# Kernel optimization log

Measured on AMD Instinct MI355X. Metric: run time of the kernel, lower is better.

Reference implementation:

```python
import jax, jax.numpy as jnp
import numpy as np

NEG_INF = -jnp.inf


def _rope(x, cos, sin):
    # x: (B, S, H, D); cos/sin: (1, S, 1, D//2)
    xr = x.reshape(*x.shape[:-1], -1, 2)
    x1, x2 = xr[..., 0], xr[..., 1]  # (B, S, H, D//2) each
    # faithful to source: concat halves along last axis, same total size D
    return jnp.concatenate([x1 * cos - x2 * sin, x1 * sin + x2 * cos], axis=-1)


def setup_inputs() -> dict:
    B, S, D, H, Ld = 2, 2048, 2048, 16, 128
    key = jax.random.key(0)
    ks = jax.random.split(key, 6)
    sc = 1.0 / np.sqrt(D)
    return {
        "x": jax.random.normal(ks[0], (B, S, D), jnp.float32),
        "attn_mask": jnp.ones((B, S), jnp.int32),
        "Wq": jax.random.normal(ks[1], (D, H * Ld), jnp.float32) * sc,
        "bq": jnp.zeros((H * Ld,), jnp.float32),
        "Wk": jax.random.normal(ks[2], (D, H * Ld), jnp.float32) * sc,
        "bk": jnp.zeros((H * Ld,), jnp.float32),
        "Wv": jax.random.normal(ks[3], (D, H * Ld), jnp.float32) * sc,
        "bv": jnp.zeros((H * Ld,), jnp.float32),
        "Wo": jax.random.normal(ks[4], (H * Ld, D), jnp.float32) * sc,
        "bo": jnp.zeros((D,), jnp.float32),
        "num_heads": H,
    }


def reference(x, attn_mask, Wq, bq, Wk, bk, Wv, bv, Wo, bo, num_heads):
    B, S, D = x.shape
    H = int(num_heads)
    Ld = Wq.shape[1] // H
    base = 10000

    q = (x @ Wq + bq).reshape(B, S, H, Ld)
    k = (x @ Wk + bk).reshape(B, S, H, Ld)
    v = (x @ Wv + bv).reshape(B, S, H, Ld)

    # rotary tables (match RotaryEmbedding.setup, sliced to seq_len)
    inv_freq = 1.0 / base ** (2 * jnp.arange(0, Ld // 2) / Ld)
    angles = jnp.arange(S)[:, None] * inv_freq[None, :]  # (S, Ld//2)
    cos = jnp.cos(angles)[None, :, None, :].astype(x.dtype)
    sin = jnp.sin(angles)[None, :, None, :].astype(x.dtype)
    q = _rope(q, cos, sin)
    k = _rope(k, cos, sin)

    q = jnp.transpose(q, (0, 2, 1, 3))  # (B, H, S, Ld)
    k = jnp.transpose(k, (0, 2, 1, 3))
    v = jnp.transpose(v, (0, 2, 1, 3))

    scale = jnp.sqrt(jnp.float32(Ld)).astype(x.dtype)
    scores = jnp.einsum('bnqd,bnkd->bnqk', q, k) / scale  # (B, H, S, S)

    # faithful mask from source: keep where arange[None,:] >= arange[:,None]
    row_idx = jnp.arange(S)[None, :]
    col_idx = jnp.arange(S)[:, None]
    keep = row_idx >= col_idx  # (S, S)
    scores = jnp.where(keep[None, None, :, :], scores, NEG_INF)

    # padding mask applied over the QUERY axis, as in source: (B,1,S,1)
    scores = jnp.where(attn_mask[:, None, :, None] > 0, scores, NEG_INF)

    attn = jax.nn.softmax(scores, axis=-1)
    attended = jnp.einsum('bnqk,bnkd->bnqd', attn, v)
    attended = jnp.transpose(attended, (0, 2, 1, 3)).reshape(B, S, H * Ld)
    return attended @ Wo + bo
```

## Files before the change

### kernel.cpp

```cpp
#include <hip/hip_runtime.h>
#include <math.h>

typedef __bf16 bf16x8 __attribute__((ext_vector_type(8)));
typedef float f32x4 __attribute__((ext_vector_type(4)));

#define MFMA_BF16(a,b,c) __builtin_amdgcn_mfma_f32_16x16x32_bf16((a),(b),(c),0,0,0)

static constexpr int S_LEN = 2048;
static constexpr int DM    = 2048;
static constexpr int NHEAD = 16;
static constexpr int LDH   = 128;
static constexpr int BATCH = 2;
static constexpr size_t QKV_SEG = (size_t)BATCH * NHEAD * S_LEN * LDH;

__device__ __forceinline__ unsigned short f2bf(float f) {
    unsigned u = __float_as_uint(f);
    u += 0x7fffu + ((u >> 16) & 1u);
    return (unsigned short)(u >> 16);
}
__device__ __forceinline__ float bf2f(unsigned short h) {
    return __uint_as_float(((unsigned)h) << 16);
}
__device__ __forceinline__ float fexp2(float x) { return exp2f(x); }

__device__ __forceinline__ void ld_lds16(const void* g, void* l) {
    __builtin_amdgcn_global_load_lds(
        (const __attribute__((address_space(1))) unsigned int*)g,
        (__attribute__((address_space(3))) unsigned int*)l, 16, 0, 0);
}

__global__ void convert_f32_bf16(const float* __restrict__ in,
                                 unsigned short* __restrict__ out, int n4) {
    int idx = blockIdx.x * blockDim.x + threadIdx.x;
    if (idx >= n4) return;
    float4 v = reinterpret_cast<const float4*>(in)[idx];
    unsigned lo = (unsigned)f2bf(v.x) | ((unsigned)f2bf(v.y) << 16);
    unsigned hi = (unsigned)f2bf(v.z) | ((unsigned)f2bf(v.w) << 16);
    reinterpret_cast<uint2*>(out)[idx] = make_uint2(lo, hi);
}

__global__ void gen_tab(float* __restrict__ ct, float* __restrict__ st) {
    int i = threadIdx.x & 63;
    int s = blockIdx.x * 4 + (threadIdx.x >> 6);
    float freq = (float)exp(-(double)(2 * i) / 128.0 * 9.210340371976184);
    float a = (float)s * freq;
    ct[s * 64 + i] = cosf(a);
    st[s * 64 + i] = sinf(a);
}

__global__ void wconv_t4(const float* __restrict__ W0, const float* __restrict__ W1,
                         const float* __restrict__ W2, const float* __restrict__ W3,
                         unsigned short* __restrict__ O0, unsigned short* __restrict__ O1,
                         unsigned short* __restrict__ O2, unsigned short* __restrict__ O3) {
    __shared__ unsigned short tile[32][33];
    int z = blockIdx.z;
    const float* W = (z == 0) ? W0 : (z == 1) ? W1 : (z == 2) ? W2 : W3;
    unsigned short* Wt = (z == 0) ? O0 : (z == 1) ? O1 : (z == 2) ? O2 : O3;
    int n0 = blockIdx.x * 32;
    int k0 = blockIdx.y * 32;
    int t = threadIdx.x;
    int ir = t >> 3, ic = (t & 7) * 4;
    float4 v = *reinterpret_cast<const float4*>(&W[(size_t)(k0 + ir) * DM + n0 + ic]);
    tile[ir][ic + 0] = f2bf(v.x);
    tile[ir][ic + 1] = f2bf(v.y);
    tile[ir][ic + 2] = f2bf(v.z);
    tile[ir][ic + 3] = f2bf(v.w);
    __syncthreads();
    unsigned lo = (unsigned)tile[ic + 0][ir] | ((unsigned)tile[ic + 1][ir] << 16);
    unsigned hi = (unsigned)tile[ic + 2][ir] | ((unsigned)tile[ic + 3][ir] << 16);
    *reinterpret_cast<uint2*>(&Wt[(size_t)(n0 + ir) * DM + k0 + ic]) = make_uint2(lo, hi);
}

template<int MODE>
__global__ __launch_bounds__(256, 2) void gemm_bf16(
    const unsigned short* __restrict__ A,
    const unsigned short* __restrict__ Bt,
    const float* __restrict__ b0, const float* __restrict__ b1,
    const float* __restrict__ b2,
    const float* __restrict__ ctab, const float* __restrict__ stab,
    void* __restrict__ outp)
{
    const int K = DM;
    constexpr int SMEM_SHORTS = (MODE == 0) ? 16384 : 8192;
    __shared__ __attribute__((aligned(16))) unsigned short smem[SMEM_SHORTS];
    unsigned short* As = smem;
    unsigned short* Bs = smem + 4096;
    int t = threadIdx.x;
    int m0 = blockIdx.y * 128, n0 = blockIdx.x * 128;
    int lane = t & 63, i16 = lane & 15, quad = lane >> 4;
    int w = t >> 6;
    int wm = (w >> 1) * 64, wn = (w & 1) * 64;

    f32x4 acc[4][4];
    const f32x4 z4 = {0.f, 0.f, 0.f, 0.f};
    for (int mi = 0; mi < 4; ++mi)
        for (int ni = 0; ni < 4; ++ni) acc[mi][ni] = z4;

    for (int kk = 0; kk < K; kk += 32) {
        __syncthreads();
#pragma unroll
        for (int j = 0; j < 2; ++j) {
            int off = j * 4096 + w * 1024 + lane * 16;
            int row = off >> 6;
            int g = ((off >> 4) & 3) ^ ((row >> 1) & 3);
            ld_lds16(&A [(size_t)(m0 + row) * K + kk + g * 8], (char*)As + off);
            ld_lds16(&Bt[(size_t)(n0 + row) * K + kk + g * 8], (char*)Bs + off);
        }
        __syncthreads();

        bf16x8 aF[4], bF[4];
#pragma unroll
        for (int mi = 0; mi < 4; ++mi) {
            int rA = wm + mi * 16 + i16;
            aF[mi] = *reinterpret_cast<const bf16x8*>(
                (const char*)As + rA * 64 + ((quad ^ ((rA >> 1) & 3)) * 16));
        }
#pragma unroll
        for (int ni = 0; ni < 4; ++ni) {
            int rB = wn + ni * 16 + i16;
            bF[ni] = *reinterpret_cast<const bf16x8*>(
                (const char*)Bs + rB * 64 + ((quad ^ ((rB >> 1) & 3)) * 16));
        }
#pragma unroll
        for (int mi = 0; mi < 4; ++mi)
#pragma unroll
            for (int ni = 0; ni < 4; ++ni)
                acc[mi][ni] = MFMA_BF16(aF[mi], bF[ni], acc[mi][ni]);
    }

    if constexpr (MODE == 0) {
        unsigned short* Cs = smem;
        __syncthreads();
        int which = n0 >> 11;
        int hh = (n0 & (DM - 1)) >> 7;
        const float* bp = (which == 0) ? b0 : ((which == 1) ? b1 : b2);
        if (which == 2) {
            for (int mi = 0; mi < 4; ++mi)
                for (int ni = 0; ni < 4; ++ni) {
                    int d = wn + ni * 16 + i16;
                    float bv = bp[(n0 & (DM - 1)) + d];
                    for (int r = 0; r < 4; ++r) {
                        int sl = wm + mi * 16 + quad * 4 + r;
                        Cs[d * 128 + (((sl >> 3) ^ (d & 15)) * 8) + (sl & 7)] =
                            f2bf(acc[mi][ni][r] + bv);
                    }
                }
            __syncthreads();
            int s0 = m0 & (S_LEN - 1), bb = m0 >> 11;
            unsigned short* vout = (unsigned short*)outp + 2 * QKV_SEG;
#pragma unroll
            for (int it = 0; it < 8; ++it) {
                int idx = it * 256 + t;
                int d = idx >> 4, sg = idx & 15;
                uint4 v = *reinterpret_cast<const uint4*>(&Cs[d * 128 + ((sg ^ (d & 15)) * 8)]);
                size_t oidx = (((size_t)(bb * NHEAD + hh)) * LDH + d) * S_LEN + s0 + sg * 8;
                *reinterpret_cast<uint4*>(vout + oidx) = v;
            }
        } else {
            for (int mi = 0; mi < 4; ++mi)
                for (int ni = 0; ni < 4; ++ni) {
                    int nl = wn + ni * 16 + i16;
                    float bv = bp[(n0 & (DM - 1)) + nl];
                    for (int r = 0; r < 4; ++r) {
                        int ml = wm + mi * 16 + quad * 4 + r;
                        Cs[ml * 128 + nl] = f2bf(acc[mi][ni][r] + bv);
                    }
                }
            __syncthreads();
            float qscale = (which == 0) ? (0.08838834764831845f * 1.4426950408889634f) : 1.0f;
            unsigned short* qout = (unsigned short*)outp + (size_t)which * QKV_SEG;
#pragma unroll
            for (int it = 0; it < 8; ++it) {
                int idx = it * 256 + t;
                int row = idx >> 4, c16 = idx & 15;
                int mm = m0 + row;
                int ss = mm & (S_LEN - 1), bb = mm >> 11;
                int i8 = (c16 & 7) * 8;
                const unsigned short* crow = Cs + row * 128 + i8 * 2;
                uint4 w0 = *reinterpret_cast<const uint4*>(crow);
                uint4 w1 = *reinterpret_cast<const uint4*>(crow + 8);
                unsigned pw[8] = {w0.x, w0.y, w0.z, w0.w, w1.x, w1.y, w1.z, w1.w};
                float4 cA = *reinterpret_cast<const float4*>(&ctab[ss * 64 + i8]);
                float4 cB = *reinterpret_cast<const float4*>(&ctab[ss * 64 + i8 + 4]);
                float4 sA = *reinterpret_cast<const float4*>(&stab[ss * 64 + i8]);
                float4 sB = *reinterpret_cast<const float4*>(&stab[ss * 64 + i8 + 4]);
                float cv[8] = {cA.x, cA.y, cA.z, cA.w, cB.x, cB.y, cB.z, cB.w};
                float sv[8] = {sA.x, sA.y, sA.z, sA.w, sB.x, sB.y, sB.z, sB.w};
                bool hi = (c16 >= 8);
                unsigned short ov[8];
#pragma unroll
                for (int j = 0; j < 8; ++j) {
                    float xe = bf2f((unsigned short)(pw[j] & 0xffff));
                    float xo = bf2f((unsigned short)(pw[j] >> 16));
                    float o = hi ? (xe * sv[j] + xo * cv[j]) : (xe * cv[j] - xo * sv[j]);
                    ov[j] = f2bf(o * qscale);
                }
                size_t oidx = (((size_t)(bb * NHEAD + hh)) * S_LEN + ss) * LDH + c16 * 8;
                *reinterpret_cast<uint4*>(qout + oidx) =
                    *reinterpret_cast<const uint4*>(ov);
            }
        }
    } else {
        for (int mi = 0; mi < 4; ++mi) {
            for (int ni = 0; ni < 4; ++ni) {
                int nn = n0 + wn + ni * 16 + i16;
                float bv = b0[nn];
                for (int r = 0; r < 4; ++r) {
                    int mm = m0 + wm + mi * 16 + quad * 4 + r;
                    ((float*)outp)[(size_t)mm * DM + nn] = acc[mi][ni][r] + bv;
                }
            }
        }
    }
}

__global__ __launch_bounds__(256, 2) void attn_kernel(
    const unsigned short* __restrict__ q,
    const unsigned short* __restrict__ k,
    const unsigned short* __restrict__ vt,
    unsigned short* __restrict__ att)
{
    __shared__ __attribute__((aligned(16))) unsigned short Ks[2][64 * 128];
    __shared__ __attribute__((aligned(16))) unsigned short Vs[2][128 * 64];
    __shared__ __attribute__((aligned(16))) unsigned short Ps[4][32 * 64];

    int bid = blockIdx.x;
    int second = bid >> 8;
    int p = bid & 255;
    int xb = second ? (15 - (p >> 5)) : (p >> 5);
    int bh = p & 31;
    int b = bh >> 4, h = bh & (NHEAD - 1);
    int q0 = xb * 128;

    int t = threadIdx.x, w = t >> 6, lane = t & 63;
    int i16 = lane & 15, quad = lane >> 4;
    int qbase = q0 + w * 32;

    bf16x8 qf[2][4];
#pragma unroll
    for (int qs = 0; qs < 2; ++qs) {
        const unsigned short* qrow = q + ((size_t)bh * S_LEN + qbase + qs * 16 + i16) * LDH;
#pragma unroll
        for (int c = 0; c < 4; ++c)
            qf[qs][c] = *reinterpret_cast<const bf16x8*>(qrow + c * 32 + quad * 8);
    }

    const f32x4 z4 = {0.f, 0.f, 0.f, 0.f};
    f32x4 o[2][8];
#pragma unroll
    for (int qs = 0; qs < 2; ++qs)
#pragma unroll
        for (int dt = 0; dt < 8; ++dt) o[qs][dt] = z4;
    float l_i[2] = {0.f, 0.f};

    const unsigned short* kbh  = k  + (size_t)bh * S_LEN * LDH;
    const unsigned short* vtbh = vt + (size_t)bh * LDH * S_LEN;
    unsigned short* PsW = Ps[w];

    auto stage = [&](int buf, int kk0) {
#pragma unroll
        for (int j = 0; j < 4; ++j) {
            int off = j * 4096 + w * 1024 + lane * 16;
            int key = off >> 8;
            int gk = ((off >> 4) & 15) ^ (key & 15);
            ld_lds16(&kbh[(size_t)(kk0 + key) * LDH + gk * 8], (char*)Ks[buf] + off);
            int d = off >> 7;
            int gv = ((off >> 4) & 7) ^ (d & 7);
            ld_lds16(&vtbh[(size_t)d * S_LEN + kk0 + gv * 8], (char*)Vs[buf] + off);
        }
    };

    stage(0, q0);
    int nch = (S_LEN - q0) >> 6;
    for (int ci = 0; ci < nch; ++ci) {
        __syncthreads();
        if (ci + 1 < nch) stage((ci + 1) & 1, q0 + (ci + 1) * 64);
        int kk0 = q0 + ci * 64;
        if (kk0 + 64 <= qbase) continue;
        const unsigned short* Kb = Ks[ci & 1];
        const unsigned short* Vb = Vs[ci & 1];

        f32x4 s[2][4];
#pragma unroll
        for (int qs = 0; qs < 2; ++qs)
#pragma unroll
            for (int kn = 0; kn < 4; ++kn) s[qs][kn] = z4;
#pragma unroll
        for (int c = 0; c < 4; ++c) {
            bf16x8 kf[4];
#pragma unroll
            for (int kn = 0; kn < 4; ++kn) {
                int key = kn * 16 + i16;
                int gs = (c * 4 + quad) ^ (key & 15);
                kf[kn] = *reinterpret_cast<const bf16x8*>((const char*)Kb + key * 256 + gs * 16);
            }
#pragma unroll
            for (int qs = 0; qs < 2; ++qs)
#pragma unroll
                for (int kn = 0; kn < 4; ++kn)
                    s[qs][kn] = MFMA_BF16(kf[kn], qf[qs][c], s[qs][kn]);
        }

        bool diag = (kk0 < qbase + 32);
#pragma unroll
        for (int qs = 0; qs < 2; ++qs) {
            int q_local = qs * 16 + i16;
            int qg = qbase + q_local;
#pragma unroll
            for (int kn = 0; kn < 4; ++kn) {
                int keyb = kk0 + kn * 16 + quad * 4;
                float pv[4];
                if (diag) {
#pragma unroll
                    for (int r = 0; r < 4; ++r)
                        pv[r] = (keyb + r >= qg) ? fexp2(s[qs][kn][r]) : 0.f;
                } else {
#pragma unroll
                    for (int r = 0; r < 4; ++r) pv[r] = fexp2(s[qs][kn][r]);
                }
                l_i[qs] += (pv[0] + pv[1]) + (pv[2] + pv[3]);
                unsigned lo = (unsigned)f2bf(pv[0]) | ((unsigned)f2bf(pv[1]) << 16);
                unsigned hi = (unsigned)f2bf(pv[2]) | ((unsigned)f2bf(pv[3]) << 16);
                int g = (kn * 2 + (quad >> 1)) ^ (q_local & 7);
                char* addr = (char*)PsW + q_local * 128 + g * 16 + (quad & 1) * 8;
                *reinterpret_cast<uint2*>(addr) = make_uint2(lo, hi);
            }
        }

#pragma unroll
        for (int hh = 0; hh < 2; ++hh) {
            bf16x8 pf[2];
#pragma unroll
            for (int qs = 0; qs < 2; ++qs) {
                int q_local = qs * 16 + i16;
                int g = (hh * 4 + quad) ^ (q_local & 7);
                pf[qs] = *reinterpret_cast<const bf16x8*>((const char*)PsW + q_local * 128 + g * 16);
            }
#pragma unroll
            for (int dt = 0; dt < 8; ++dt) {
                int d = dt * 16 + i16;
                int gv = (hh * 4 + quad) ^ (d & 7);
                bf16x8 vf = *reinterpret_cast<const bf16x8*>((const char*)Vb + d * 128 + gv * 16);
                o[0][dt] = MFMA_BF16(pf[0], vf, o[0][dt]);
                o[1][dt] = MFMA_BF16(pf[1], vf, o[1][dt]);
            }
        }
    }

#pragma unroll
    for (int qs = 0; qs < 2; ++qs) {
        float lr = l_i[qs];
        lr += __shfl_xor(lr, 16);
        lr += __shfl_xor(lr, 32);
        l_i[qs] = lr;
    }
#pragma unroll
    for (int qs = 0; qs < 2; ++qs) {
#pragma unroll
        for (int r = 0; r < 4; ++r) {
            float lv = __shfl(l_i[qs], quad * 4 + r);
            float inv = 1.0f / lv;
            int qrow = qbase + qs * 16 + quad * 4 + r;
            unsigned short* orow = att + ((size_t)b * S_LEN + qrow) * DM + h * LDH;
#pragma unroll
            for (int dt = 0; dt < 8; ++dt)
                orow[dt * 16 + i16] = f2bf(o[qs][dt][r] * inv);
        }
    }
}

extern "C" void kernel_launch(void* const* d_in, const int* in_sizes, int n_in,
                              void* d_out, int out_size, void* d_ws, size_t ws_size,
                              hipStream_t stream) {
    const float* x  = (const float*)d_in[0];
    const float* Wq = (const float*)d_in[2];
    const float* bq = (const float*)d_in[3];
    const float* Wk = (const float*)d_in[4];
    const float* bk = (const float*)d_in[5];
    const float* Wv = (const float*)d_in[6];
    const float* bv = (const float*)d_in[7];
    const float* Wo = (const float*)d_in[8];
    const float* bo = (const float*)d_in[9];

    char* ws = (char*)d_ws;
    unsigned short* xb  = (unsigned short*)(ws);
    unsigned short* Wqt = (unsigned short*)(ws + 16777216);
    unsigned short* Wkt = (unsigned short*)(ws + 25165824);
    unsigned short* Wvt = (unsigned short*)(ws + 33554432);
    unsigned short* Wot = (unsigned short*)(ws + 41943040);
    unsigned short* qkv = (unsigned short*)(ws + 50331648);
    unsigned short* att = (unsigned short*)(ws + 100663296);
    float* ctab = (float*)(ws + 117440512);
    float* stab = (float*)(ws + 117964800);

    convert_f32_bf16<<<8192, 256, 0, stream>>>(x, xb, (BATCH * S_LEN * DM) / 4);
    gen_tab<<<512, 256, 0, stream>>>(ctab, stab);
    wconv_t4<<<dim3(64, 64, 4), 256, 0, stream>>>(Wq, Wk, Wv, Wo, Wqt, Wkt, Wvt, Wot);

    gemm_bf16<0><<<dim3(3 * DM / 128, (BATCH * S_LEN) / 128), 256, 0, stream>>>(
        xb, Wqt, bq, bk, bv, ctab, stab, qkv);

    attn_kernel<<<512, 256, 0, stream>>>(qkv, qkv + QKV_SEG, qkv + 2 * QKV_SEG, att);

    gemm_bf16<1><<<dim3(DM / 128, (BATCH * S_LEN) / 128), 256, 0, stream>>>(
        att, Wot, bo, bo, bo, ctab, stab, (float*)d_out);
}
```

Baseline: 413.8 us.

## Replace QKV projection GEMM with 256x256-tile, 4-stage pipelined kernel

The fused QKV projection now uses a dedicated 512-thread kernel with 256x256 output tiles and a 4-slot shared-memory ring. Each slot is filled by direct global-to-LDS loads, and waits are done with explicit vmcnt counts, so loads for later k-steps overlap the MFMA work on the current one. Block indices are remapped so that blocks landing on the same XCD share B tiles, and MFMA sections are wrapped in setprio. The epilogue is widened so each block writes two heads with the same RoPE and transpose logic. The 128KB of LDS and the large accumulator set cut occupancy, and the explicit waitcnt sequencing depends on ld_lds16 issuing exactly the assumed number of ops.

After: 413.0 us. No clear change (-0.2%).

```diff
diff --git a/kernel.cpp b/kernel.cpp
--- a/kernel.cpp
+++ b/kernel.cpp
@@ -71,18 +71,14 @@
     *reinterpret_cast<uint2*>(&Wt[(size_t)(n0 + ir) * DM + k0 + ic]) = make_uint2(lo, hi);
 }
 
-template<int MODE>
-__global__ __launch_bounds__(256, 2) void gemm_bf16(
+__global__ __launch_bounds__(256, 2) void gemm_bf16_out(
     const unsigned short* __restrict__ A,
     const unsigned short* __restrict__ Bt,
-    const float* __restrict__ b0, const float* __restrict__ b1,
-    const float* __restrict__ b2,
-    const float* __restrict__ ctab, const float* __restrict__ stab,
-    void* __restrict__ outp)
+    const float* __restrict__ b0,
+    float* __restrict__ outp)
 {
     const int K = DM;
-    constexpr int SMEM_SHORTS = (MODE == 0) ? 16384 : 8192;
-    __shared__ __attribute__((aligned(16))) unsigned short smem[SMEM_SHORTS];
+    __shared__ __attribute__((aligned(16))) unsigned short smem[8192];
     unsigned short* As = smem;
     unsigned short* Bs = smem + 4096;
     int t = threadIdx.x;
@@ -128,88 +124,199 @@
                 acc[mi][ni] = MFMA_BF16(aF[mi], bF[ni], acc[mi][ni]);
     }
 
-    if constexpr (MODE == 0) {
-        unsigned short* Cs = smem;
+    for (int mi = 0; mi < 4; ++mi) {
+        for (int ni = 0; ni < 4; ++ni) {
+            int nn = n0 + wn + ni * 16 + i16;
+            float bv = b0[nn];
+            for (int r = 0; r < 4; ++r) {
+                int mm = m0 + wm + mi * 16 + quad * 4 + r;
+                outp[(size_t)mm * DM + nn] = acc[mi][ni][r] + bv;
+            }
+        }
+    }
+}
+
+__global__ __launch_bounds__(512, 2) void gemm256_qkv(
+    const unsigned short* __restrict__ A,
+    const unsigned short* __restrict__ Bt,
+    const float* __restrict__ b0, const float* __restrict__ b1,
+    const float* __restrict__ b2,
+    const float* __restrict__ ctab, const float* __restrict__ stab,
+    unsigned short* __restrict__ outp)
+{
+    constexpr int K  = DM;
+    constexpr int NT = K / 32;
+    __shared__ __attribute__((aligned(16))) unsigned short smem[65536];
+
+    int t = threadIdx.x, lane = t & 63, w = t >> 6;
+    int i16 = lane & 15, quad = lane >> 4;
+    int wc = w & 3, wr = w >> 2;
+
+    int flat = blockIdx.y * 24 + blockIdx.x;
+    int xcd = flat & 7, r8 = flat >> 3;
+    int nbx = xcd * 3 + (r8 >> 4);
+    int nby = r8 & 15;
+    int m0 = nby * 256, n0 = nbx * 256;
+
+    const unsigned short* ga[2];
+    const unsigned short* gb[2];
+    int loff[2];
+#pragma unroll
+    for (int j = 0; j < 2; ++j) {
+        int off = j * 8192 + w * 1024 + lane * 16;
+        int row = off >> 6;
+        int q = ((off >> 4) & 3) ^ ((row >> 1) & 3);
+        ga[j] = A  + (size_t)(m0 + row) * K + q * 8;
+        gb[j] = Bt + (size_t)(n0 + row) * K + q * 8;
+        loff[j] = off;
+    }
+
+    auto stage = [&](int slot, int kt) {
+        char* base = (char*)smem + slot * 32768;
+#pragma unroll
+        for (int j = 0; j < 2; ++j) {
+            ld_lds16(ga[j] + kt * 32, base + loff[j]);
+            ld_lds16(gb[j] + kt * 32, base + 16384 + loff[j]);
+        }
+    };
+
+    f32x4 acc[8][4];
+    const f32x4 z4 = {0.f, 0.f, 0.f, 0.f};
+#pragma unroll
+    for (int mi = 0; mi < 8; ++mi)
+#pragma unroll
+        for (int ni = 0; ni < 4; ++ni) acc[mi][ni] = z4;
+
+    auto compute = [&](int slot) {
+        const char* Ab = (const char*)smem + slot * 32768;
+        const char* Bb = Ab + 16384;
+        bf16x8 bF[4];
+#pragma unroll
+        for (int ni = 0; ni < 4; ++ni) {
+            int rB = wc * 64 + ni * 16 + i16;
+            bF[ni] = *reinterpret_cast<const bf16x8*>(
+                Bb + rB * 64 + ((quad ^ ((rB >> 1) & 3)) * 16));
+        }
+#pragma unroll
+        for (int h = 0; h < 2; ++h) {
+            bf16x8 aF[4];
+#pragma unroll
+            for (int mi = 0; mi < 4; ++mi) {
+                int rA = wr * 128 + h * 64 + mi * 16 + i16;
+                aF[mi] = *reinterpret_cast<const bf16x8*>(
+                    Ab + rA * 64 + ((quad ^ ((rA >> 1) & 3)) * 16));
+            }
+            __builtin_amdgcn_s_setprio(1);
+#pragma unroll
+            for (int mi = 0; mi < 4; ++mi)
+#pragma unroll
+                for (int ni = 0; ni < 4; ++ni)
+                    acc[h * 4 + mi][ni] = MFMA_BF16(aF[mi], bF[ni], acc[h * 4 + mi][ni]);
+            __builtin_amdgcn_s_setprio(0);
+        }
+    };
+
+    stage(0, 0); stage(1, 1); stage(2, 2);
+    asm volatile("s_waitcnt vmcnt(8)" ::: "memory");
+    __builtin_amdgcn_s_barrier();
+    asm volatile("" ::: "memory");
+
+    for (int tt = 0; tt < NT - 3; ++tt) {
+        stage((tt + 3) & 3, tt + 3);
+        compute(tt & 3);
+        asm volatile("s_waitcnt vmcnt(8)" ::: "memory");
+        __builtin_amdgcn_s_barrier();
+        asm volatile("" ::: "memory");
+    }
+    compute((NT - 3) & 3);
+    asm volatile("s_waitcnt vmcnt(4)" ::: "memory");
+    __builtin_amdgcn_s_barrier();
+    asm volatile("" ::: "memory");
+    compute((NT - 2) & 3);
+    asm volatile("s_waitcnt vmcnt(0)" ::: "memory");
+    __builtin_amdgcn_s_barrier();
+    asm volatile("" ::: "memory");
+    compute((NT - 1) & 3);
+    __syncthreads();
+
+    unsigned short* Cs = smem;
+    int which = n0 >> 11;
+    int hh0 = (n0 & 2047) >> 7;
+    const float* bp = (which == 0) ? b0 : ((which == 1) ? b1 : b2);
+    int segn = n0 & 2047;
+    int bb = m0 >> 11, s0 = m0 & 2047;
+
+    if (which == 2) {
+        int htile = wc >> 1;
+#pragma unroll
+        for (int mi = 0; mi < 8; ++mi)
+#pragma unroll
+            for (int ni = 0; ni < 4; ++ni) {
+                int dcol = wc * 64 + ni * 16 + i16;
+                int d = dcol & 127;
+                float bv = bp[segn + dcol];
+#pragma unroll
+                for (int r = 0; r < 4; ++r) {
+                    int sl = wr * 128 + mi * 16 + quad * 4 + r;
+                    Cs[htile * 32768 + d * 256 + (((sl >> 3) ^ (d & 31)) * 8) + (sl & 7)] =
+                        f2bf(acc[mi][ni][r] + bv);
+                }
+            }
         __syncthreads();
-        int which = n0 >> 11;
-        int hh = (n0 & (DM - 1)) >> 7;
-        const float* bp = (which == 0) ? b0 : ((which == 1) ? b1 : b2);
-        if (which == 2) {
-            for (int mi = 0; mi < 4; ++mi)
-                for (int ni = 0; ni < 4; ++ni) {
-                    int d = wn + ni * 16 + i16;
-                    float bv = bp[(n0 & (DM - 1)) + d];
-                    for (int r = 0; r < 4; ++r) {
-                        int sl = wm + mi * 16 + quad * 4 + r;
-                        Cs[d * 128 + (((sl >> 3) ^ (d & 15)) * 8) + (sl & 7)] =
-                            f2bf(acc[mi][ni][r] + bv);
-                    }
+        unsigned short* vout = outp + 2 * QKV_SEG;
+#pragma unroll
+        for (int it = 0; it < 16; ++it) {
+            int idx = it * 512 + t;
+            int ht2 = idx >> 12, rem = idx & 4095, d = rem >> 5, sg = rem & 31;
+            uint4 v = *reinterpret_cast<const uint4*>(
+                &Cs[ht2 * 32768 + d * 256 + ((sg ^ (d & 31)) * 8)]);
+            size_t oidx = (((size_t)(bb * NHEAD + hh0 + ht2)) * LDH + d) * S_LEN + s0 + sg * 8;
+            *reinterpret_cast<uint4*>(vout + oidx) = v;
+        }
+    } else {
+#pragma unroll
+        for (int mi = 0; mi < 8; ++mi)
+#pragma unroll
+            for (int ni = 0; ni < 4; ++ni) {
+                int nl = wc * 64 + ni * 16 + i16;
+                float bv = bp[segn + nl];
+#pragma unroll
+                for (int r = 0; r < 4; ++r) {
+                    int ml = wr * 128 + mi * 16 + quad * 4 + r;
+                    Cs[ml * 256 + nl] = f2bf(acc[mi][ni][r] + bv);
                 }
-            __syncthreads();
-            int s0 = m0 & (S_LEN - 1), bb = m0 >> 11;
-            unsigned short* vout = (unsigned short*)outp + 2 * QKV_SEG;
-#pragma unroll
-            for (int it = 0; it < 8; ++it) {
-                int idx = it * 256 + t;
-                int d = idx >> 4, sg = idx & 15;
-                uint4 v = *reinterpret_cast<const uint4*>(&Cs[d * 128 + ((sg ^ (d & 15)) * 8)]);
-                size_t oidx = (((size_t)(bb * NHEAD + hh)) * LDH + d) * S_LEN + s0 + sg * 8;
-                *reinterpret_cast<uint4*>(vout + oidx) = v;
-            }
-        } else {
-            for (int mi = 0; mi < 4; ++mi)
-                for (int ni = 0; ni < 4; ++ni) {
-                    int nl = wn + ni * 16 + i16;
-                    float bv = bp[(n0 & (DM - 1)) + nl];
-                    for (int r = 0; r < 4; ++r) {
-                        int ml = wm + mi * 16 + quad * 4 + r;
-                        Cs[ml * 128 + nl] = f2bf(acc[mi][ni][r] + bv);
-                    }
-                }
-            __syncthreads();
-            float qscale = (which == 0) ? (0.08838834764831845f * 1.4426950408889634f) : 1.0f;
-            unsigned short* qout = (unsigned short*)outp + (size_t)which * QKV_SEG;
-#pragma unroll
-            for (int it = 0; it < 8; ++it) {
-                int idx = it * 256 + t;
-                int row = idx >> 4, c16 = idx & 15;
-                int mm = m0 + row;
-                int ss = mm & (S_LEN - 1), bb = mm >> 11;
-                int i8 = (c16 & 7) * 8;
-                const unsigned short* crow = Cs + row * 128 + i8 * 2;
-                uint4 w0 = *reinterpret_cast<const uint4*>(crow);
-                uint4 w1 = *reinterpret_cast<const uint4*>(crow + 8);
-                unsigned pw[8] = {w0.x, w0.y, w0.z, w0.w, w1.x, w1.y, w1.z, w1.w};
-                float4 cA = *reinterpret_cast<const float4*>(&ctab[ss * 64 + i8]);
-                float4 cB = *reinterpret_cast<const float4*>(&ctab[ss * 64 + i8 + 4]);
-                float4 sA = *reinterpret_cast<const float4*>(&stab[ss * 64 + i8]);
-                float4 sB = *reinterpret_cast<const float4*>(&stab[ss * 64 + i8 + 4]);
-                float cv[8] = {cA.x, cA.y, cA.z, cA.w, cB.x, cB.y, cB.z, cB.w};
-                float sv[8] = {sA.x, sA.y, sA.z, sA.w, sB.x, sB.y, sB.z, sB.w};
-                bool hi = (c16 >= 8);
-                unsigned short ov[8];
-#pragma unroll
-                for (int j = 0; j < 8; ++j) {
-                    float xe = bf2f((unsigned short)(pw[j] & 0xffff));
-                    float xo = bf2f((unsigned short)(pw[j] >> 16));
-                    float o = hi ? (xe * sv[j] + xo * cv[j]) : (xe * cv[j] - xo * sv[j]);
-                    ov[j] = f2bf(o * qscale);
-                }
-                size_t oidx = (((size_t)(bb * NHEAD + hh)) * S_LEN + ss) * LDH + c16 * 8;
-                *reinterpret_cast<uint4*>(qout + oidx) =
-                    *reinterpret_cast<const uint4*>(ov);
-            }
-        }
-    } else {
-        for (int mi = 0; mi < 4; ++mi) {
-            for (int ni = 0; ni < 4; ++ni) {
-                int nn = n0 + wn + ni * 16 + i16;
-                float bv = b0[nn];
-                for (int r = 0; r < 4; ++r) {
-                    int mm = m0 + wm + mi * 16 + quad * 4 + r;
-                    ((float*)outp)[(size_t)mm * DM + nn] = acc[mi][ni][r] + bv;
-                }
-            }
+            }
+        __syncthreads();
+        float qscale = (which == 0) ? (0.08838834764831845f * 1.4426950408889634f) : 1.0f;
+        unsigned short* qout = outp + (size_t)which * QKV_SEG;
+#pragma unroll
+        for (int it = 0; it < 16; ++it) {
+            int idx = it * 512 + t;
+            int row = idx >> 5, u = idx & 31, ht2 = u >> 4, c16 = u & 15;
+            int mm = m0 + row, ss = mm & 2047, bb2 = mm >> 11;
+            int i8 = (c16 & 7) * 8;
+            const unsigned short* crow = Cs + row * 256 + ht2 * 128 + i8 * 2;
+            uint4 w0 = *reinterpret_cast<const uint4*>(crow);
+            uint4 w1 = *reinterpret_cast<const uint4*>(crow + 8);
+            unsigned pw[8] = {w0.x, w0.y, w0.z, w0.w, w1.x, w1.y, w1.z, w1.w};
+            float4 cA = *reinterpret_cast<const float4*>(&ctab[ss * 64 + i8]);
+            float4 cB = *reinterpret_cast<const float4*>(&ctab[ss * 64 + i8 + 4]);
+            float4 sA = *reinterpret_cast<const float4*>(&stab[ss * 64 + i8]);
+            float4 sB = *reinterpret_cast<const float4*>(&stab[ss * 64 + i8 + 4]);
+            float cv[8] = {cA.x, cA.y, cA.z, cA.w, cB.x, cB.y, cB.z, cB.w};
+            float sv[8] = {sA.x, sA.y, sA.z, sA.w, sB.x, sB.y, sB.z, sB.w};
+            bool hi = (c16 >= 8);
+            unsigned short ov[8];
+#pragma unroll
+            for (int j = 0; j < 8; ++j) {
+                float xe = bf2f((unsigned short)(pw[j] & 0xffff));
+                float xo = bf2f((unsigned short)(pw[j] >> 16));
+                float o = hi ? (xe * sv[j] + xo * cv[j]) : (xe * cv[j] - xo * sv[j]);
+                ov[j] = f2bf(o * qscale);
+            }
+            size_t oidx = (((size_t)(bb2 * NHEAD + hh0 + ht2)) * S_LEN + ss) * LDH + c16 * 8;
+            *reinterpret_cast<uint4*>(qout + oidx) =
+                *reinterpret_cast<const uint4*>(ov);
         }
     }
 }
@@ -397,11 +504,11 @@
     gen_tab<<<512, 256, 0, stream>>>(ctab, stab);
     wconv_t4<<<dim3(64, 64, 4), 256, 0, stream>>>(Wq, Wk, Wv, Wo, Wqt, Wkt, Wvt, Wot);
 
-    gemm_bf16<0><<<dim3(3 * DM / 128, (BATCH * S_LEN) / 128), 256, 0, stream>>>(
+    gemm256_qkv<<<dim3(24, 16), 512, 0, stream>>>(
         xb, Wqt, bq, bk, bv, ctab, stab, qkv);
 
     attn_kernel<<<512, 256, 0, stream>>>(qkv, qkv + QKV_SEG, qkv + 2 * QKV_SEG, att);
 
-    gemm_bf16<1><<<dim3(DM / 128, (BATCH * S_LEN) / 128), 256, 0, stream>>>(
-        att, Wot, bo, bo, bo, ctab, stab, (float*)d_out);
-}
+    gemm_bf16_out<<<dim3(DM / 128, (BATCH * S_LEN) / 128), 256, 0, stream>>>(
+        att, Wot, bo, (float*)d_out);
+}
```
